# Kernel tuning notes

Hardware: AMD Instinct MI355X
Metric: run time of the kernel (lower is better)

Reference implementation:

```python
import jax, jax.numpy as jnp
import numpy as np

KERNEL_SIZE = 5


def setup_inputs() -> dict:
    key = jax.random.key(0)
    k1, k2 = jax.random.split(key)
    x = jax.random.normal(k1, (4, 32, 256, 256), dtype=jnp.float32)
    kernel = jax.random.normal(k2, (4, KERNEL_SIZE * KERNEL_SIZE, 256, 256), dtype=jnp.float32)
    return {"x": x, "kernel": kernel}


def reference(x, kernel):
    k = KERNEL_SIZE
    b, kk, h, w = kernel.shape
    # softmax over the k*k dim (original permutes to channels-last then softmax dim=-1)
    kern = jax.nn.softmax(jnp.transpose(kernel, (0, 2, 3, 1)), axis=-1)  # [b,h,w,k*k]
    pad = (k - 1) // 2
    # replicate padding on spatial dims
    xp = jnp.pad(x, ((0, 0), (0, 0), (pad, pad), (pad, pad)), mode="edge")
    # unfold: patch index order is di*k + dj (height offset first), matching torch unfold(2).unfold(3)
    patches = jnp.stack(
        [xp[:, :, i:i + h, j:j + w] for i in range(k) for j in range(k)], axis=-1
    )  # [b,c,h,w,k*k]
    # per-pixel softmax-weighted local sum; kernel broadcast over channel dim
    out = jnp.sum(patches * kern[:, None, :, :, :], axis=-1)  # [b,c,h,w]
    return out
```

## Files before the change

kernel.cpp:

```cpp
#include <hip/hip_runtime.h>

#define HW    256
#define HW2   (HW*HW)
#define C     32
#define CPB   8

__global__ __launch_bounds__(256, 5) void ddown_kernel(
    const float* __restrict__ x,
    const float* __restrict__ kern,
    float* __restrict__ out)
{
    const int t   = threadIdx.x;
    const int txq = t & 15;
    const int ty  = t >> 4;
    const int w0  = blockIdx.x * 32;
    const int h0  = blockIdx.y * 16;
    const int b   = blockIdx.z >> 2;
    const int c0  = (blockIdx.z & 3) * CPB;

    const int h = h0 + ty;
    const int c = w0 + txq * 2;

    const float* kb = kern + (size_t)b * 25 * HW2 + h * HW + c;
    float2 wt[25];
    float sx = 0.f, sy = 0.f;
#pragma unroll
    for (int j = 0; j < 25; ++j) {
        float2 v = *(const float2*)(kb + (size_t)j * HW2);
        v.x = __expf(v.x); v.y = __expf(v.y);
        sx += v.x; sy += v.y;
        wt[j] = v;
    }
    const float ix = 1.f / sx, iy = 1.f / sy;

    int row_off[5];
#pragma unroll
    for (int di = 0; di < 5; ++di) {
        int hr = h - 2 + di;
        hr = min(max(hr, 0), HW - 1);
        row_off[di] = hr * HW;
    }
    int p0 = (c - 2) / 2; p0 = min(max(p0, 0), HW / 2 - 1);
    int p1 = c / 2;
    int p2 = (c + 2) / 2; p2 = min(max(p2, 0), HW / 2 - 1);
    const int cp0 = p0 * 2, cp1 = p1 * 2, cp2 = p2 * 2;
    const bool lfix = (c == 0);
    const bool rfix = (c == HW - 2);

    const float* xc = x + (size_t)(b * C + c0) * HW2;
    float*       ob = out + (size_t)(b * C + c0) * HW2 + h * HW + c;

    for (int cc = 0; cc < CPB; ++cc) {
        float a0 = 0.f, a1 = 0.f;
#pragma unroll
        for (int di = 0; di < 5; ++di) {
            const float* r = xc + row_off[di];
            float2 qa = *(const float2*)(r + cp0);
            float2 qb = *(const float2*)(r + cp1);
            float2 qc = *(const float2*)(r + cp2);
            float e0 = qa.x;
            float e1 = lfix ? qa.x : qa.y;
            float e2 = qb.x, e3 = qb.y;
            float e4 = rfix ? qc.y : qc.x;
            float e5 = qc.y;

            float2 t0 = wt[di * 5 + 0];
            float2 t1 = wt[di * 5 + 1];
            float2 t2 = wt[di * 5 + 2];
            float2 t3 = wt[di * 5 + 3];
            float2 t4 = wt[di * 5 + 4];
            a0 += t0.x * e0 + t1.x * e1 + t2.x * e2 + t3.x * e3 + t4.x * e4;
            a1 += t0.y * e1 + t1.y * e2 + t2.y * e3 + t3.y * e4 + t4.y * e5;
        }
        float2 res = { a0 * ix, a1 * iy };
        *(float2*)ob = res;
        xc += HW2;
        ob += HW2;
    }
}

extern "C" void kernel_launch(void* const* d_in, const int* in_sizes, int n_in,
                              void* d_out, int out_size, void* d_ws, size_t ws_size,
                              hipStream_t stream) {
    const float* x    = (const float*)d_in[0];
    const float* kern = (const float*)d_in[1];
    float* out        = (float*)d_out;

    dim3 grid(HW / 32, HW / 16, 4 * 4);
    ddown_kernel<<<grid, 256, 0, stream>>>(x, kern, out);
}
```

Before: 128.8 us.

## Double-buffer channel input tiles in registers and prefetch before softmax weights

```diff
diff --git a/kernel.cpp b/kernel.cpp
--- a/kernel.cpp
+++ b/kernel.cpp
@@ -5,7 +5,7 @@
 #define C     32
 #define CPB   8
 
-__global__ __launch_bounds__(256, 5) void ddown_kernel(
+__global__ __launch_bounds__(256, 4) void ddown_kernel(
     const float* __restrict__ x,
     const float* __restrict__ kern,
     float* __restrict__ out)
@@ -21,6 +21,35 @@
     const int h = h0 + ty;
     const int c = w0 + txq * 2;
 
+    int row_off[5];
+#pragma unroll
+    for (int di = 0; di < 5; ++di) {
+        int hr = h - 2 + di;
+        hr = min(max(hr, 0), HW - 1);
+        row_off[di] = hr * HW;
+    }
+    int p0 = (c - 2) / 2; p0 = min(max(p0, 0), HW / 2 - 1);
+    int p2 = (c + 2) / 2; p2 = min(max(p2, 0), HW / 2 - 1);
+    const int cp0 = p0 * 2, cp1 = c, cp2 = p2 * 2;
+    const bool lfix = (c == 0);
+    const bool rfix = (c == HW - 2);
+
+    const float* xc = x + (size_t)(b * C + c0) * HW2;
+
+    float2 A0[5], B0[5], Q0[5], A1[5], B1[5], Q1[5];
+
+    auto load_tile = [&](float2* A, float2* B, float2* Q, const float* xb) {
+#pragma unroll
+        for (int di = 0; di < 5; ++di) {
+            const float* r = xb + row_off[di];
+            A[di] = *(const float2*)(r + cp0);
+            B[di] = *(const float2*)(r + cp1);
+            Q[di] = *(const float2*)(r + cp2);
+        }
+    };
+
+    load_tile(A0, B0, Q0, xc);
+
     const float* kb = kern + (size_t)b * 25 * HW2 + h * HW + c;
     float2 wt[25];
     float sx = 0.f, sy = 0.f;
@@ -33,49 +62,41 @@
     }
     const float ix = 1.f / sx, iy = 1.f / sy;
 
-    int row_off[5];
-#pragma unroll
-    for (int di = 0; di < 5; ++di) {
-        int hr = h - 2 + di;
-        hr = min(max(hr, 0), HW - 1);
-        row_off[di] = hr * HW;
-    }
-    int p0 = (c - 2) / 2; p0 = min(max(p0, 0), HW / 2 - 1);
-    int p1 = c / 2;
-    int p2 = (c + 2) / 2; p2 = min(max(p2, 0), HW / 2 - 1);
-    const int cp0 = p0 * 2, cp1 = p1 * 2, cp2 = p2 * 2;
-    const bool lfix = (c == 0);
-    const bool rfix = (c == HW - 2);
+    float* ob = out + (size_t)(b * C + c0) * HW2 + h * HW + c;
 
-    const float* xc = x + (size_t)(b * C + c0) * HW2;
-    float*       ob = out + (size_t)(b * C + c0) * HW2 + h * HW + c;
-
-    for (int cc = 0; cc < CPB; ++cc) {
-        float a0 = 0.f, a1 = 0.f;
+    auto compute_store = [&](const float2* A, const float2* B, const float2* Q,
+                             float* o) {
+        float a0 = 0.f, a1 = 0.f, d0 = 0.f, d1 = 0.f;
 #pragma unroll
         for (int di = 0; di < 5; ++di) {
-            const float* r = xc + row_off[di];
-            float2 qa = *(const float2*)(r + cp0);
-            float2 qb = *(const float2*)(r + cp1);
-            float2 qc = *(const float2*)(r + cp2);
-            float e0 = qa.x;
-            float e1 = lfix ? qa.x : qa.y;
-            float e2 = qb.x, e3 = qb.y;
-            float e4 = rfix ? qc.y : qc.x;
-            float e5 = qc.y;
-
+            float e0 = A[di].x;
+            float e1 = lfix ? A[di].x : A[di].y;
+            float e2 = B[di].x, e3 = B[di].y;
+            float e4 = rfix ? Q[di].y : Q[di].x;
+            float e5 = Q[di].y;
             float2 t0 = wt[di * 5 + 0];
             float2 t1 = wt[di * 5 + 1];
             float2 t2 = wt[di * 5 + 2];
             float2 t3 = wt[di * 5 + 3];
             float2 t4 = wt[di * 5 + 4];
-            a0 += t0.x * e0 + t1.x * e1 + t2.x * e2 + t3.x * e3 + t4.x * e4;
-            a1 += t0.y * e1 + t1.y * e2 + t2.y * e3 + t3.y * e4 + t4.y * e5;
+            a0 += t0.x * e0 + t1.x * e1 + t2.x * e2;
+            d0 += t3.x * e3 + t4.x * e4;
+            a1 += t0.y * e1 + t1.y * e2 + t2.y * e3;
+            d1 += t3.y * e4 + t4.y * e5;
         }
-        float2 res = { a0 * ix, a1 * iy };
-        *(float2*)ob = res;
-        xc += HW2;
-        ob += HW2;
+        float2 res = { (a0 + d0) * ix, (a1 + d1) * iy };
+        *(float2*)o = res;
+    };
+
+#pragma unroll
+    for (int cc = 0; cc < CPB; cc += 2) {
+        load_tile(A1, B1, Q1, xc + HW2);
+        compute_store(A0, B0, Q0, ob);
+        if (cc + 2 < CPB)
+            load_tile(A0, B0, Q0, xc + 2 * HW2);
+        compute_store(A1, B1, Q1, ob + HW2);
+        xc += 2 * HW2;
+        ob += 2 * HW2;
     }
 }
 
```

After: 125.2 us. 1.03x faster.
